# Optimization experiments

Measured on AMD Instinct MI355X. Metric: run time of the kernel, lower is better.

Reference implementation:

```python
import jax, jax.numpy as jnp
import numpy as np

EPS = float(jnp.finfo(jnp.float32).eps)  # torch.nn.RMSNorm default eps for fp32
TOP_K = 2


def rmsnorm(x, w):
    return x * jax.lax.rsqrt(jnp.mean(x * x, axis=-1, keepdims=True) + EPS) * w


def setup_inputs() -> dict:
    B, T, D_IN, D_MODEL, D_FF, D_OUT, E = 8, 1024, 1024, 1024, 4096, 1024, 8
    STD = 0.02
    key = jax.random.key(0)
    ks = jax.random.split(key, 8)
    return {
        "s": jax.random.normal(ks[0], (B, T, D_IN), dtype=jnp.float32),
        "W_in": STD * jax.random.normal(ks[1], (D_MODEL, D_IN), dtype=jnp.float32),
        "in_norm_w": jnp.ones((D_MODEL,), dtype=jnp.float32),
        "Wr": STD * jax.random.normal(ks[2], (E, D_MODEL), dtype=jnp.float32),
        "expert_bias": jnp.zeros((E,), dtype=jnp.float32),
        "Wg": STD * jax.random.normal(ks[3], (E, D_FF, D_MODEL), dtype=jnp.float32),
        "Wu": STD * jax.random.normal(ks[4], (E, D_FF, D_MODEL), dtype=jnp.float32),
        "Wd": STD * jax.random.normal(ks[5], (E, D_MODEL, D_FF), dtype=jnp.float32),
        "enorm_w": jnp.ones((E, D_MODEL), dtype=jnp.float32),
        "out_norm_w": jnp.ones((D_MODEL,), dtype=jnp.float32),
        "W_out": STD * jax.random.normal(ks[6], (D_OUT, D_MODEL), dtype=jnp.float32),
    }


def reference(s, W_in, in_norm_w, Wr, expert_bias, Wg, Wu, Wd, enorm_w, out_norm_w, W_out):
    B, T, _ = s.shape
    x = s.reshape(B * T, -1)                      # (N, d_in)
    h = rmsnorm(x @ W_in.T, in_norm_w)            # (N, d_model)

    # --- top-k router (DeepSeek-style bias for selection, orig logits for gates) ---
    logits = h @ Wr.T                              # (N, E)
    _, idx = jax.lax.top_k(logits + expert_bias, TOP_K)   # (N, k)
    sel = jnp.take_along_axis(logits, idx, axis=-1)
    g_topk = jax.nn.softmax(sel, axis=-1)
    N = logits.shape[0]
    gates = jnp.zeros_like(logits).at[jnp.arange(N)[:, None], idx].set(g_topk)

    # --- experts: gates are exactly 0 for unselected experts, so the dense
    # weighted sum equals the original masked gather/scatter combine ---
    out = jnp.zeros_like(h)
    for e in range(Wg.shape[0]):
        gate = jax.nn.silu(h @ Wg[e].T)            # (N, d_ff)
        up = h @ Wu[e].T
        oe = rmsnorm((gate * up) @ Wd[e].T, enorm_w[e])
        out = out + gates[:, e:e + 1] * oe

    s_hat = rmsnorm(out, out_norm_w) @ W_out.T     # (N, d_out)
    return s_hat.reshape(B, T, -1)
```

## Files before the change

### kernel.cpp

```cpp
#include <hip/hip_runtime.h>


#define NT      8192
#define DMODEL  1024
#define DFF     4096
#define NEXP    8
#define MAXROWS (NT * 2 + NEXP * 256)
#define RMS_EPS 1.1920928955078125e-07f

typedef __attribute__((ext_vector_type(8))) short bf16x8;
typedef __attribute__((ext_vector_type(4))) float f32x4;

__device__ __forceinline__ float bf2f(unsigned short u) {
  union { unsigned int i; float f; } c; c.i = ((unsigned int)u) << 16; return c.f;
}
__device__ __forceinline__ unsigned short f2bf(float f) {
  union { float f; unsigned int i; } c; c.f = f;
  unsigned int x = c.i;
  return (unsigned short)((x + 0x7FFFu + ((x >> 16) & 1u)) >> 16);
}

#define BARX() __builtin_amdgcn_s_barrier()
#define LGKM0() do { asm volatile("s_waitcnt lgkmcnt(0)" ::: "memory"); \
                     __builtin_amdgcn_sched_barrier(0); } while (0)
#define VMC(n)  do { asm volatile("s_waitcnt vmcnt(" #n ")" ::: "memory"); \
                     __builtin_amdgcn_sched_barrier(0); } while (0)

__global__ __launch_bounds__(256) void cast_bf16_kernel(
    const float* __restrict__ src, unsigned short* __restrict__ dst, long n) {
  long i = ((long)blockIdx.x * 256 + threadIdx.x) * 4;
  const long stride = (long)gridDim.x * 1024;
  for (; i < n; i += stride) {
    float4 v = *(const float4*)(src + i);
    ushort4 o;
    o.x = f2bf(v.x); o.y = f2bf(v.y); o.z = f2bf(v.z); o.w = f2bf(v.w);
    *(ushort4*)(dst + i) = o;
  }
}

__device__ __forceinline__ void async_cp16(const void* g, void* l) {
  __builtin_amdgcn_global_load_lds((const __attribute__((address_space(1))) void*)g,
                                   (__attribute__((address_space(3))) void*)l, 16, 0, 0);
}

template <int FUSED>
__global__ __launch_bounds__(512, 2) void gemm8ph(
    const unsigned short* __restrict__ A,
    const unsigned short* __restrict__ W0,
    const unsigned short* __restrict__ W1,
    void* __restrict__ Cv, void* __restrict__ Cv2,
    const int* __restrict__ offs,
    int K, int KT, size_t wstride) {
  const int gx = gridDim.x;
  const int nwg = gx * gridDim.y;
  int bid = blockIdx.y * gx + blockIdx.x;
  {
    const int q = nwg >> 3, r = nwg & 7;
    const int x = bid & 7, l = bid >> 3;
    bid = (x < r ? x * (q + 1) : r * (q + 1) + (x - r) * q) + l;
  }
  const int bx = bid % gx, by = bid / gx;

  const int row0 = bx * 256;
  if (row0 >= offs[NEXP]) return;
  int e = 0;
#pragma unroll
  for (int i = 1; i < NEXP; ++i) e += (row0 >= offs[i]) ? 1 : 0;

  __shared__ __align__(16) unsigned short lds[65536];

  const int t = threadIdx.x;
  const int lane = t & 63;
  const int wave = t >> 6;
  const int wm = wave >> 2, wn = wave & 3;
  const int lm = lane & 15, kq = lane >> 4;
  const int k0 = blockIdx.z * (KT << 6);

  const unsigned short* aP[2];
  const unsigned short* bP[2];
  int dl[2];
#pragma unroll
  for (int q = 0; q < 2; ++q) {
    const int L = q * 512 + t;
    const int row = L >> 2;
    const int kp = (t & 3) ^ ((row >> 1) & 3);
    dl[q] = L * 8;
    aP[q] = A + (size_t)(row0 + row) * K + kp * 8 + k0;
    if (FUSED) {
      const int f = by * 128 + ((row >> 6) << 5) + (row & 31);
      const unsigned short* wb = (row & 32) ? W1 : W0;
      bP[q] = wb + (size_t)e * wstride + (size_t)f * K + kp * 8 + k0;
    } else {
      bP[q] = W0 + (size_t)e * wstride + (size_t)(by * 256 + row) * K + kp * 8 + k0;
    }
  }

  int afo[8], bfo[4];
#pragma unroll
  for (int mi = 0; mi < 8; ++mi) {
    const int r = wm * 128 + mi * 16 + lm;
    afo[mi] = r * 32 + ((kq ^ ((r >> 1) & 3)) << 3);
  }
#pragma unroll
  for (int ni = 0; ni < 4; ++ni) {
    const int r = wn * 64 + ni * 16 + lm;
    bfo[ni] = 16384 + r * 32 + ((kq ^ ((r >> 1) & 3)) << 3);
  }

  f32x4 acc[8][4];
#pragma unroll
  for (int i = 0; i < 8; ++i)
#pragma unroll
    for (int j = 0; j < 4; ++j) acc[i][j] = (f32x4){0.f, 0.f, 0.f, 0.f};

  auto STG = [&](int tau, int ks, int isB) {
    const int roff = ((tau & 1) << 15) + (isB << 14) + (ks << 13);
    const int koff = (tau << 6) + (ks << 5);
#pragma unroll
    for (int q = 0; q < 2; ++q)
      async_cp16((isB ? bP[q] : aP[q]) + koff, lds + roff + dl[q]);
  };

  STG(0, 0, 0); STG(0, 0, 1); STG(0, 1, 0); STG(0, 1, 1);
  STG(1, 0, 0); STG(1, 0, 1); STG(1, 1, 0);
  VMC(6);
  BARX();

  for (int tau = 0; tau < KT; ++tau) {
    const int tb = (tau & 1) << 15;
    const bool s1 = (tau + 1 < KT), s2 = (tau + 2 < KT);
    bf16x8 af[8], bq0, bq1;

#pragma unroll
    for (int mi = 0; mi < 8; ++mi) af[mi] = *(const bf16x8*)(lds + tb + afo[mi]);
    bq0 = *(const bf16x8*)(lds + tb + bfo[0]);
    bq1 = *(const bf16x8*)(lds + tb + bfo[1]);
    if (s1) STG(tau + 1, 1, 1);
    BARX(); LGKM0();
    __builtin_amdgcn_s_setprio(1);
#pragma unroll
    for (int mi = 0; mi < 8; ++mi) {
      acc[mi][0] = __builtin_amdgcn_mfma_f32_16x16x32_bf16(af[mi], bq0, acc[mi][0], 0, 0, 0);
      acc[mi][1] = __builtin_amdgcn_mfma_f32_16x16x32_bf16(af[mi], bq1, acc[mi][1], 0, 0, 0);
    }
    __builtin_amdgcn_s_setprio(0);
    BARX();

    bq0 = *(const bf16x8*)(lds + tb + bfo[2]);
    bq1 = *(const bf16x8*)(lds + tb + bfo[3]);
    if (s2) STG(tau + 2, 0, 0);
    BARX(); LGKM0();
    __builtin_amdgcn_s_setprio(1);
#pragma unroll
    for (int mi = 0; mi < 8; ++mi) {
      acc[mi][2] = __builtin_amdgcn_mfma_f32_16x16x32_bf16(af[mi], bq0, acc[mi][2], 0, 0, 0);
      acc[mi][3] = __builtin_amdgcn_mfma_f32_16x16x32_bf16(af[mi], bq1, acc[mi][3], 0, 0, 0);
    }
    __builtin_amdgcn_s_setprio(0);
    BARX();

#pragma unroll
    for (int mi = 0; mi < 8; ++mi) af[mi] = *(const bf16x8*)(lds + tb + 8192 + afo[mi]);
    bq0 = *(const bf16x8*)(lds + tb + 8192 + bfo[0]);
    bq1 = *(const bf16x8*)(lds + tb + 8192 + bfo[1]);
    if (s2) STG(tau + 2, 0, 1);
    BARX(); LGKM0();
    __builtin_amdgcn_s_setprio(1);
#pragma unroll
    for (int mi = 0; mi < 8; ++mi) {
      acc[mi][0] = __builtin_amdgcn_mfma_f32_16x16x32_bf16(af[mi], bq0, acc[mi][0], 0, 0, 0);
      acc[mi][1] = __builtin_amdgcn_mfma_f32_16x16x32_bf16(af[mi], bq1, acc[mi][1], 0, 0, 0);
    }
    __builtin_amdgcn_s_setprio(0);
    BARX();

    bq0 = *(const bf16x8*)(lds + tb + 8192 + bfo[2]);
    bq1 = *(const bf16x8*)(lds + tb + 8192 + bfo[3]);
    if (s2) STG(tau + 2, 1, 0);
    BARX(); LGKM0();
    __builtin_amdgcn_s_setprio(1);
#pragma unroll
    for (int mi = 0; mi < 8; ++mi) {
      acc[mi][2] = __builtin_amdgcn_mfma_f32_16x16x32_bf16(af[mi], bq0, acc[mi][2], 0, 0, 0);
      acc[mi][3] = __builtin_amdgcn_mfma_f32_16x16x32_bf16(af[mi], bq1, acc[mi][3], 0, 0, 0);
    }
    __builtin_amdgcn_s_setprio(0);
    if (tau + 3 <= KT) { VMC(6); }
    else if (tau + 2 == KT) { VMC(0); }
    BARX();
  }

  const long rbase = (long)row0 + wm * 128 + kq * 4;
  if (FUSED) {
    unsigned short* Hc = (unsigned short*)Cv;
    const int cb = by * 128 + wn * 32 + lm;
#pragma unroll
    for (int mi = 0; mi < 8; ++mi)
#pragma unroll
      for (int ni = 0; ni < 2; ++ni)
#pragma unroll
        for (int rr = 0; rr < 4; ++rr) {
          const float g = acc[mi][ni][rr];
          const float u = acc[mi][ni + 2][rr];
          const float h = g / (1.f + expf(-g)) * u;
          Hc[(rbase + mi * 16 + rr) * (long)DFF + cb + ni * 16] = f2bf(h);
        }
  } else {
    float* Cp = blockIdx.z ? (float*)Cv2 : (float*)Cv;
    const int cb = by * 256 + wn * 64 + lm;
#pragma unroll
    for (int mi = 0; mi < 8; ++mi)
#pragma unroll
      for (int ni = 0; ni < 4; ++ni)
#pragma unroll
        for (int rr = 0; rr < 4; ++rr)
          Cp[(rbase + mi * 16 + rr) * (long)DMODEL + cb + ni * 16] = acc[mi][ni][rr];
  }
}

template <int BM, int BN, int WM, int WN, int WRITE_BF16, int FUSE_SILU, int GROUPED>
__global__ __launch_bounds__(WM * WN * 64, 2) void gemm2ph(
    const unsigned short* __restrict__ A,
    const unsigned short* __restrict__ W,
    void* __restrict__ Cv,
    const int* __restrict__ offs,
    int N, int K, size_t wstride) {
  constexpr int NTHR = WM * WN * 64;
  constexpr int TM = BM / WM;
  constexpr int TN = BN / WN;
  constexpr int AM = TM / 16;
  constexpr int AN = TN / 16;
  constexpr int LA = BM * 8 / NTHR;
  constexpr int LB = BN * 8 / NTHR;

  const int gx = gridDim.x;
  const int nwg = gx * gridDim.y;
  int bid = blockIdx.y * gx + blockIdx.x;
  {
    const int q = nwg >> 3, r = nwg & 7;
    const int x = bid & 7, l = bid >> 3;
    bid = (x < r ? x * (q + 1) : r * (q + 1) + (x - r) * q) + l;
  }
  const int bx = bid % gx;
  const int by = bid / gx;

  const int row0 = bx * BM;
  const unsigned short* Bp;
  if constexpr (GROUPED) {
    if (row0 >= offs[NEXP]) return;
    int e = 0;
#pragma unroll
    for (int i = 1; i < NEXP; ++i) e += (row0 >= offs[i]) ? 1 : 0;
    Bp = W + (size_t)e * wstride;
  } else {
    Bp = W;
  }

  __shared__ __align__(16) unsigned short As[2][BM * 64];
  __shared__ __align__(16) unsigned short Bs[2][BN * 64];

  const int tid = threadIdx.x;
  const int lane = tid & 63, wave = tid >> 6;
  const int wm = wave / WN, wn = wave % WN;
  const int lm = lane & 15, kq = lane >> 4;

  const long arow = row0;
  const long brow = (long)by * BN;

  const unsigned short* asrc[LA];
  unsigned short* adst[LA];
#pragma unroll
  for (int q = 0; q < LA; ++q) {
    const int c = q * NTHR + tid;
    asrc[q] = A + (arow + (c >> 3)) * (long)K + ((c & 7) << 3);
    adst[q] = &As[0][c * 8];
  }
  const unsigned short* bsrc[LB];
  unsigned short* bdst[LB];
#pragma unroll
  for (int q = 0; q < LB; ++q) {
    const int c = q * NTHR + tid;
    bsrc[q] = Bp + (brow + (c >> 3)) * (long)K + ((c & 7) << 3);
    bdst[q] = &Bs[0][c * 8];
  }

  f32x4 acc[AM][AN];
#pragma unroll
  for (int i = 0; i < AM; ++i)
#pragma unroll
    for (int j = 0; j < AN; ++j) acc[i][j] = (f32x4){0.f, 0.f, 0.f, 0.f};

  const int KT = K >> 6;

#pragma unroll
  for (int q = 0; q < LA; ++q) async_cp16(asrc[q], adst[q]);
#pragma unroll
  for (int q = 0; q < LB; ++q) async_cp16(bsrc[q], bdst[q]);
  __syncthreads();

  for (int kt = 0; kt < KT; ++kt) {
    const int cur = kt & 1;
    if (kt + 1 < KT) {
      const int koff = (kt + 1) << 6;
      const int ao = (cur ^ 1) * (BM * 64);
      const int bo = (cur ^ 1) * (BN * 64);
#pragma unroll
      for (int q = 0; q < LA; ++q) async_cp16(asrc[q] + koff, adst[q] + ao);
#pragma unroll
      for (int q = 0; q < LB; ++q) async_cp16(bsrc[q] + koff, bdst[q] + bo);
    }
    const unsigned short* Ab = As[cur];
    const unsigned short* Bb = Bs[cur];
#pragma unroll
    for (int ks = 0; ks < 2; ++ks) {
      bf16x8 af[AM], bfr[AN];
#pragma unroll
      for (int mi = 0; mi < AM; ++mi)
        af[mi] = *(const bf16x8*)(Ab + (wm * TM + mi * 16 + lm) * 64 + ks * 32 + kq * 8);
#pragma unroll
      for (int ni = 0; ni < AN; ++ni)
        bfr[ni] = *(const bf16x8*)(Bb + (wn * TN + ni * 16 + lm) * 64 + ks * 32 + kq * 8);
#pragma unroll
      for (int mi = 0; mi < AM; ++mi)
#pragma unroll
        for (int ni = 0; ni < AN; ++ni)
          acc[mi][ni] = __builtin_amdgcn_mfma_f32_16x16x32_bf16(af[mi], bfr[ni],
                                                                acc[mi][ni], 0, 0, 0);
    }
    __syncthreads();
  }

  const long rbase = arow + wm * TM + kq * 4;
  const long cbase = brow + wn * TN + lm;
#pragma unroll
  for (int mi = 0; mi < AM; ++mi)
#pragma unroll
    for (int ni = 0; ni < AN; ++ni)
#pragma unroll
      for (int r = 0; r < 4; ++r) {
        const long row = rbase + mi * 16 + r;
        const long col = cbase + ni * 16;
        float v = acc[mi][ni][r];
        if constexpr (FUSE_SILU) {
          const float g = bf2f(((const unsigned short*)Cv)[row * N + col]);
          v = g / (1.f + expf(-g)) * v;
        }
        if constexpr (WRITE_BF16) ((unsigned short*)Cv)[row * N + col] = f2bf(v);
        else                      ((float*)Cv)[row * N + col] = v;
      }
}

__global__ __launch_bounds__(256) void rmsnorm_kernel(
    const float* __restrict__ in, const float* __restrict__ w,
    unsigned short* __restrict__ out, float* __restrict__ invrms) {
  const int row = blockIdx.x;
  const int tid = threadIdx.x;
  const float4 xv = ((const float4*)(in + (long)row * DMODEL))[tid];
  float ss = xv.x * xv.x + xv.y * xv.y + xv.z * xv.z + xv.w * xv.w;
#pragma unroll
  for (int o = 32; o > 0; o >>= 1) ss += __shfl_xor(ss, o);
  __shared__ float red[4];
  if ((tid & 63) == 0) red[tid >> 6] = ss;
  __syncthreads();
  const float tot = red[0] + red[1] + red[2] + red[3];
  const float s = rsqrtf(tot * (1.f / DMODEL) + RMS_EPS);
  if (invrms != nullptr && tid == 0) invrms[row] = s;
  const float4 wv = ((const float4*)w)[tid];
  ushort4 o4;
  o4.x = f2bf(xv.x * s * wv.x);
  o4.y = f2bf(xv.y * s * wv.y);
  o4.z = f2bf(xv.z * s * wv.z);
  o4.w = f2bf(xv.w * s * wv.w);
  ((ushort4*)(out + (long)row * DMODEL))[tid] = o4;
}

__global__ __launch_bounds__(256) void router_prep_kernel(
    const float* __restrict__ Wr, const float* __restrict__ nw,
    const float* __restrict__ W_in, float* __restrict__ Wr2) {
  __shared__ float wr[NEXP * DMODEL];
  const int tid = threadIdx.x;
  for (int i = tid; i < NEXP * DMODEL; i += 256) wr[i] = Wr[i] * nw[i & (DMODEL - 1)];
  __syncthreads();
  const int kl = tid & 127;
  const int eb = (tid >> 7) * 4;
  const int kg = blockIdx.x * 128 + kl;
  float a0 = 0.f, a1 = 0.f, a2 = 0.f, a3 = 0.f;
  for (int j = 0; j < DMODEL; ++j) {
    const float wij = W_in[(long)j * DMODEL + kg];
    a0 += wr[(eb + 0) * DMODEL + j] * wij;
    a1 += wr[(eb + 1) * DMODEL + j] * wij;
    a2 += wr[(eb + 2) * DMODEL + j] * wij;
    a3 += wr[(eb + 3) * DMODEL + j] * wij;
  }
  Wr2[(eb + 0) * DMODEL + kg] = a0;
  Wr2[(eb + 1) * DMODEL + kg] = a1;
  Wr2[(eb + 2) * DMODEL + kg] = a2;
  Wr2[(eb + 3) * DMODEL + kg] = a3;
}

__global__ __launch_bounds__(64) void router_kernel(
    const float* __restrict__ x, const float* __restrict__ Wr2,
    const float* __restrict__ bias, const float* __restrict__ invrms,
    int* __restrict__ cnt, int* __restrict__ tok, float* __restrict__ gv) {
  const int row = blockIdx.x;
  const int lane = threadIdx.x;
  const float* xr = x + (long)row * DMODEL;
  float p[NEXP] = {0.f, 0.f, 0.f, 0.f, 0.f, 0.f, 0.f, 0.f};
  for (int k = lane; k < DMODEL; k += 64) {
    const float xv = xr[k];
#pragma unroll
    for (int e = 0; e < NEXP; ++e) p[e] += xv * Wr2[e * DMODEL + k];
  }
#pragma unroll
  for (int o = 32; o > 0; o >>= 1)
#pragma unroll
    for (int e = 0; e < NEXP; ++e) p[e] += __shfl_xor(p[e], o);
  if (lane == 0) {
    const float s = invrms[row];
    float logit[NEXP];
    float b0 = -1e30f, b1 = -1e30f;
    int i0 = 0, i1 = 0;
#pragma unroll
    for (int e = 0; e < NEXP; ++e) {
      logit[e] = p[e] * s;
      const float be = logit[e] + bias[e];
      if (be > b0)      { b1 = b0; i1 = i0; b0 = be; i0 = e; }
      else if (be > b1) { b1 = be; i1 = e; }
    }
    const float l0 = logit[i0], l1 = logit[i1];
    const float m = fmaxf(l0, l1);
    const float e0 = expf(l0 - m), e1 = expf(l1 - m);
    const float inv = 1.f / (e0 + e1);
    const int s0 = atomicAdd(&cnt[i0], 1);
    tok[i0 * NT + s0] = row;
    gv[i0 * NT + s0] = e0 * inv;
    const int s1 = atomicAdd(&cnt[i1], 1);
    tok[i1 * NT + s1] = row;
    gv[i1 * NT + s1] = e1 * inv;
  }
}

__global__ __launch_bounds__(256) void pad_kernel(
    const int* __restrict__ cnt, int* __restrict__ tok,
    int* __restrict__ pcnt, int* __restrict__ off) {
  __shared__ int sc[NEXP], sp[NEXP];
  const int tid = threadIdx.x;
  if (tid == 0) {
    int o = 0;
    for (int e = 0; e < NEXP; ++e) {
      const int c = cnt[e];
      const int p = (c + 255) & ~255;
      sc[e] = c; sp[e] = p;
      pcnt[e] = p; off[e] = o;
      o += p;
    }
    off[NEXP] = o;
  }
  __syncthreads();
  for (int e = 0; e < NEXP; ++e) {
    const int c = sc[e], p = sp[e];
    for (int s = c + tid; s < p; s += 256) tok[e * NT + s] = 0;
  }
}

__global__ __launch_bounds__(256) void gather_kernel(
    const unsigned short* __restrict__ hb, const int* __restrict__ tok,
    const int* __restrict__ offs, unsigned short* __restrict__ Ac) {
  const int r = blockIdx.x;
  if (r >= offs[NEXP]) return;
  int e = 0;
#pragma unroll
  for (int i = 1; i < NEXP; ++i) e += (r >= offs[i]) ? 1 : 0;
  const int src = tok[e * NT + (r - offs[e])];
  const ushort4* s4 = (const ushort4*)(hb + (long)src * DMODEL);
  ushort4* d4 = (ushort4*)(Ac + (long)r * DMODEL);
  d4[threadIdx.x] = s4[threadIdx.x];
}

__global__ __launch_bounds__(256) void expert_scatter(
    const float* __restrict__ oe0, const float* __restrict__ oe1,
    const float* __restrict__ enw,
    const int* __restrict__ tok, const float* __restrict__ gv,
    const int* __restrict__ cnt, const int* __restrict__ off,
    int e, float* __restrict__ acc) {
  const int s = blockIdx.x;
  if (s >= cnt[e]) return;
  const int row = tok[e * NT + s];
  const float g = gv[e * NT + s];
  const int tid = threadIdx.x;
  const long idx = ((long)off[e] + s) * DMODEL;
  const float4 x0 = ((const float4*)(oe0 + idx))[tid];
  const float4 x1 = ((const float4*)(oe1 + idx))[tid];
  float4 xv;
  xv.x = x0.x + x1.x; xv.y = x0.y + x1.y; xv.z = x0.z + x1.z; xv.w = x0.w + x1.w;
  float ss = xv.x * xv.x + xv.y * xv.y + xv.z * xv.z + xv.w * xv.w;
#pragma unroll
  for (int o = 32; o > 0; o >>= 1) ss += __shfl_xor(ss, o);
  __shared__ float red[4];
  if ((tid & 63) == 0) red[tid >> 6] = ss;
  __syncthreads();
  const float tot = red[0] + red[1] + red[2] + red[3];
  const float sc = rsqrtf(tot * (1.f / DMODEL) + RMS_EPS) * g;
  const float4 wv = ((const float4*)enw)[tid];
  float4* ap = (float4*)(acc + (long)row * DMODEL) + tid;
  float4 a = *ap;
  a.x += xv.x * sc * wv.x;
  a.y += xv.y * sc * wv.y;
  a.z += xv.z * sc * wv.z;
  a.w += xv.w * sc * wv.w;
  *ap = a;
}

extern "C" void kernel_launch(void* const* d_in, const int* in_sizes, int n_in,
                              void* d_out, int out_size, void* d_ws, size_t ws_size,
                              hipStream_t stream) {
  (void)in_sizes; (void)n_in; (void)out_size; (void)ws_size;
  const float* s_in  = (const float*)d_in[0];
  const float* W_in  = (const float*)d_in[1];
  const float* innw  = (const float*)d_in[2];
  const float* Wr    = (const float*)d_in[3];
  const float* ebias = (const float*)d_in[4];
  const float* Wg    = (const float*)d_in[5];
  const float* Wu    = (const float*)d_in[6];
  const float* Wd    = (const float*)d_in[7];
  const float* enw   = (const float*)d_in[8];
  const float* outnw = (const float*)d_in[9];
  const float* W_out = (const float*)d_in[10];
  float* out = (float*)d_out;

  char* base = (char*)d_ws;
  size_t off_b = 0;
  auto alloc = [&](size_t bytes) -> char* {
    char* p = base + off_b;
    off_b += (bytes + 255) & ~(size_t)255;
    return p;
  };
  unsigned short* xb    = (unsigned short*)alloc((size_t)NT * DMODEL * 2);
  unsigned short* Winb  = (unsigned short*)alloc((size_t)DMODEL * DMODEL * 2);
  unsigned short* Wgb   = (unsigned short*)alloc((size_t)NEXP * DFF * DMODEL * 2);
  unsigned short* Wub   = (unsigned short*)alloc((size_t)NEXP * DFF * DMODEL * 2);
  unsigned short* Wdb   = (unsigned short*)alloc((size_t)NEXP * DMODEL * DFF * 2);
  unsigned short* Woutb = (unsigned short*)alloc((size_t)DMODEL * DMODEL * 2);
  float*          hpre  = (float*)alloc((size_t)NT * DMODEL * 4);
  unsigned short* hb    = (unsigned short*)alloc((size_t)NT * DMODEL * 2);
  float*          invr  = (float*)alloc((size_t)NT * 4);
  float*          Wr2   = (float*)alloc((size_t)NEXP * DMODEL * 4);
  int*            cnt   = (int*)alloc((size_t)NEXP * 4);
  int*            pcnt  = (int*)alloc((size_t)NEXP * 4);
  int*            offs  = (int*)alloc((size_t)(NEXP + 1) * 4);
  int*            tok   = (int*)alloc((size_t)NEXP * NT * 4);
  float*          gv    = (float*)alloc((size_t)NEXP * NT * 4);
  unsigned short* Ac    = (unsigned short*)alloc((size_t)MAXROWS * DMODEL * 2);
  unsigned short* Hc    = (unsigned short*)alloc((size_t)MAXROWS * DFF * 2);
  float*          oec   = (float*)alloc((size_t)MAXROWS * DMODEL * 4);
  float*          accb  = hpre;
  unsigned short* yb    = xb;
  float*          oec2  = (float*)Wgb;

  hipMemsetAsync(cnt, 0, NEXP * 4, stream);
  cast_bf16_kernel<<<2048, 256, 0, stream>>>(s_in, xb, (long)NT * DMODEL);
  cast_bf16_kernel<<<2048, 256, 0, stream>>>(W_in, Winb, (long)DMODEL * DMODEL);
  cast_bf16_kernel<<<2048, 256, 0, stream>>>(Wg, Wgb, (long)NEXP * DFF * DMODEL);
  cast_bf16_kernel<<<2048, 256, 0, stream>>>(Wu, Wub, (long)NEXP * DFF * DMODEL);
  cast_bf16_kernel<<<2048, 256, 0, stream>>>(Wd, Wdb, (long)NEXP * DMODEL * DFF);
  cast_bf16_kernel<<<2048, 256, 0, stream>>>(W_out, Woutb, (long)DMODEL * DMODEL);

  gemm2ph<128, 128, 2, 2, 0, 0, 0><<<dim3(NT / 128, DMODEL / 128), 256, 0, stream>>>(
      xb, Winb, hpre, nullptr, DMODEL, DMODEL, 0);
  rmsnorm_kernel<<<NT, 256, 0, stream>>>(hpre, innw, hb, invr);
  hipMemsetAsync(accb, 0, (size_t)NT * DMODEL * 4, stream);

  router_prep_kernel<<<DMODEL / 128, 256, 0, stream>>>(Wr, innw, W_in, Wr2);
  router_kernel<<<NT, 64, 0, stream>>>(s_in, Wr2, ebias, invr, cnt, tok, gv);
  pad_kernel<<<1, 256, 0, stream>>>(cnt, tok, pcnt, offs);

  gather_kernel<<<MAXROWS, 256, 0, stream>>>(hb, tok, offs, Ac);

  gemm8ph<1><<<dim3(MAXROWS / 256, DFF / 128), 512, 0, stream>>>(
      Ac, Wgb, Wub, Hc, nullptr, offs, DMODEL, DMODEL / 64, (size_t)DFF * DMODEL);

  gemm8ph<0><<<dim3(MAXROWS / 256, DMODEL / 256, 2), 512, 0, stream>>>(
      Hc, Wdb, nullptr, oec, oec2, offs, DFF, 32, (size_t)DMODEL * DFF);

  for (int e = 0; e < NEXP; ++e)
    expert_scatter<<<NT, 256, 0, stream>>>(
        oec, oec2, enw + (size_t)e * DMODEL, tok, gv, cnt, offs, e, accb);

  rmsnorm_kernel<<<NT, 256, 0, stream>>>(accb, outnw, yb, nullptr);
  gemm2ph<128, 128, 2, 2, 0, 0, 0><<<dim3(NT / 128, DMODEL / 128), 256, 0, stream>>>(
      yb, Woutb, out, nullptr, DMODEL, DMODEL, 0);
}
```

Baseline: 1.416 ms.

## Fuse per-expert scatter and output RMSNorm into one per-token combine kernel

Replaces the eight per-expert scatter launches, the accumulator memset and the separate output RMSNorm with one combine kernel per token. The router now records each token's expert ids, slots and gates, so the combine kernel can gather its two expert rows and apply both norms in a single pass. This removes repeated read-modify-write traffic on the fp32 accumulator. The dense input and output projections also move from the 128x128 gemm2ph kernel to the 256-tile 8-wave gemm8ph kernel with grouping disabled. Using gemm8ph with z=0 means the full K range is handled, with KT=16 for K=1024.

```diff
diff --git a/kernel.cpp b/kernel.cpp
--- a/kernel.cpp
+++ b/kernel.cpp
@@ -43,7 +43,7 @@
                                    (__attribute__((address_space(3))) void*)l, 16, 0, 0);
 }
 
-template <int FUSED>
+template <int FUSED, int GROUPED>
 __global__ __launch_bounds__(512, 2) void gemm8ph(
     const unsigned short* __restrict__ A,
     const unsigned short* __restrict__ W0,
@@ -62,10 +62,12 @@
   const int bx = bid % gx, by = bid / gx;
 
   const int row0 = bx * 256;
-  if (row0 >= offs[NEXP]) return;
   int e = 0;
-#pragma unroll
-  for (int i = 1; i < NEXP; ++i) e += (row0 >= offs[i]) ? 1 : 0;
+  if constexpr (GROUPED) {
+    if (row0 >= offs[NEXP]) return;
+#pragma unroll
+    for (int i = 1; i < NEXP; ++i) e += (row0 >= offs[i]) ? 1 : 0;
+  }
 
   __shared__ __align__(16) unsigned short lds[65536];
 
@@ -218,138 +220,6 @@
   }
 }
 
-template <int BM, int BN, int WM, int WN, int WRITE_BF16, int FUSE_SILU, int GROUPED>
-__global__ __launch_bounds__(WM * WN * 64, 2) void gemm2ph(
-    const unsigned short* __restrict__ A,
-    const unsigned short* __restrict__ W,
-    void* __restrict__ Cv,
-    const int* __restrict__ offs,
-    int N, int K, size_t wstride) {
-  constexpr int NTHR = WM * WN * 64;
-  constexpr int TM = BM / WM;
-  constexpr int TN = BN / WN;
-  constexpr int AM = TM / 16;
-  constexpr int AN = TN / 16;
-  constexpr int LA = BM * 8 / NTHR;
-  constexpr int LB = BN * 8 / NTHR;
-
-  const int gx = gridDim.x;
-  const int nwg = gx * gridDim.y;
-  int bid = blockIdx.y * gx + blockIdx.x;
-  {
-    const int q = nwg >> 3, r = nwg & 7;
-    const int x = bid & 7, l = bid >> 3;
-    bid = (x < r ? x * (q + 1) : r * (q + 1) + (x - r) * q) + l;
-  }
-  const int bx = bid % gx;
-  const int by = bid / gx;
-
-  const int row0 = bx * BM;
-  const unsigned short* Bp;
-  if constexpr (GROUPED) {
-    if (row0 >= offs[NEXP]) return;
-    int e = 0;
-#pragma unroll
-    for (int i = 1; i < NEXP; ++i) e += (row0 >= offs[i]) ? 1 : 0;
-    Bp = W + (size_t)e * wstride;
-  } else {
-    Bp = W;
-  }
-
-  __shared__ __align__(16) unsigned short As[2][BM * 64];
-  __shared__ __align__(16) unsigned short Bs[2][BN * 64];
-
-  const int tid = threadIdx.x;
-  const int lane = tid & 63, wave = tid >> 6;
-  const int wm = wave / WN, wn = wave % WN;
-  const int lm = lane & 15, kq = lane >> 4;
-
-  const long arow = row0;
-  const long brow = (long)by * BN;
-
-  const unsigned short* asrc[LA];
-  unsigned short* adst[LA];
-#pragma unroll
-  for (int q = 0; q < LA; ++q) {
-    const int c = q * NTHR + tid;
-    asrc[q] = A + (arow + (c >> 3)) * (long)K + ((c & 7) << 3);
-    adst[q] = &As[0][c * 8];
-  }
-  const unsigned short* bsrc[LB];
-  unsigned short* bdst[LB];
-#pragma unroll
-  for (int q = 0; q < LB; ++q) {
-    const int c = q * NTHR + tid;
-    bsrc[q] = Bp + (brow + (c >> 3)) * (long)K + ((c & 7) << 3);
-    bdst[q] = &Bs[0][c * 8];
-  }
-
-  f32x4 acc[AM][AN];
-#pragma unroll
-  for (int i = 0; i < AM; ++i)
-#pragma unroll
-    for (int j = 0; j < AN; ++j) acc[i][j] = (f32x4){0.f, 0.f, 0.f, 0.f};
-
-  const int KT = K >> 6;
-
-#pragma unroll
-  for (int q = 0; q < LA; ++q) async_cp16(asrc[q], adst[q]);
-#pragma unroll
-  for (int q = 0; q < LB; ++q) async_cp16(bsrc[q], bdst[q]);
-  __syncthreads();
-
-  for (int kt = 0; kt < KT; ++kt) {
-    const int cur = kt & 1;
-    if (kt + 1 < KT) {
-      const int koff = (kt + 1) << 6;
-      const int ao = (cur ^ 1) * (BM * 64);
-      const int bo = (cur ^ 1) * (BN * 64);
-#pragma unroll
-      for (int q = 0; q < LA; ++q) async_cp16(asrc[q] + koff, adst[q] + ao);
-#pragma unroll
-      for (int q = 0; q < LB; ++q) async_cp16(bsrc[q] + koff, bdst[q] + bo);
-    }
-    const unsigned short* Ab = As[cur];
-    const unsigned short* Bb = Bs[cur];
-#pragma unroll
-    for (int ks = 0; ks < 2; ++ks) {
-      bf16x8 af[AM], bfr[AN];
-#pragma unroll
-      for (int mi = 0; mi < AM; ++mi)
-        af[mi] = *(const bf16x8*)(Ab + (wm * TM + mi * 16 + lm) * 64 + ks * 32 + kq * 8);
-#pragma unroll
-      for (int ni = 0; ni < AN; ++ni)
-        bfr[ni] = *(const bf16x8*)(Bb + (wn * TN + ni * 16 + lm) * 64 + ks * 32 + kq * 8);
-#pragma unroll
-      for (int mi = 0; mi < AM; ++mi)
-#pragma unroll
-        for (int ni = 0; ni < AN; ++ni)
-          acc[mi][ni] = __builtin_amdgcn_mfma_f32_16x16x32_bf16(af[mi], bfr[ni],
-                                                                acc[mi][ni], 0, 0, 0);
-    }
-    __syncthreads();
-  }
-
-  const long rbase = arow + wm * TM + kq * 4;
-  const long cbase = brow + wn * TN + lm;
-#pragma unroll
-  for (int mi = 0; mi < AM; ++mi)
-#pragma unroll
-    for (int ni = 0; ni < AN; ++ni)
-#pragma unroll
-      for (int r = 0; r < 4; ++r) {
-        const long row = rbase + mi * 16 + r;
-        const long col = cbase + ni * 16;
-        float v = acc[mi][ni][r];
-        if constexpr (FUSE_SILU) {
-          const float g = bf2f(((const unsigned short*)Cv)[row * N + col]);
-          v = g / (1.f + expf(-g)) * v;
-        }
-        if constexpr (WRITE_BF16) ((unsigned short*)Cv)[row * N + col] = f2bf(v);
-        else                      ((float*)Cv)[row * N + col] = v;
-      }
-}
-
 __global__ __launch_bounds__(256) void rmsnorm_kernel(
     const float* __restrict__ in, const float* __restrict__ w,
     unsigned short* __restrict__ out, float* __restrict__ invrms) {
@@ -401,7 +271,8 @@
 __global__ __launch_bounds__(64) void router_kernel(
     const float* __restrict__ x, const float* __restrict__ Wr2,
     const float* __restrict__ bias, const float* __restrict__ invrms,
-    int* __restrict__ cnt, int* __restrict__ tok, float* __restrict__ gv) {
+    int* __restrict__ cnt, int* __restrict__ tok,
+    int* __restrict__ te, int2* __restrict__ ts, float2* __restrict__ tg) {
   const int row = blockIdx.x;
   const int lane = threadIdx.x;
   const float* xr = x + (long)row * DMODEL;
@@ -433,16 +304,16 @@
     const float inv = 1.f / (e0 + e1);
     const int s0 = atomicAdd(&cnt[i0], 1);
     tok[i0 * NT + s0] = row;
-    gv[i0 * NT + s0] = e0 * inv;
     const int s1 = atomicAdd(&cnt[i1], 1);
     tok[i1 * NT + s1] = row;
-    gv[i1 * NT + s1] = e1 * inv;
+    te[row] = i0 | (i1 << 8);
+    ts[row] = make_int2(s0, s1);
+    tg[row] = make_float2(e0 * inv, e1 * inv);
   }
 }
 
 __global__ __launch_bounds__(256) void pad_kernel(
-    const int* __restrict__ cnt, int* __restrict__ tok,
-    int* __restrict__ pcnt, int* __restrict__ off) {
+    const int* __restrict__ cnt, int* __restrict__ tok, int* __restrict__ off) {
   __shared__ int sc[NEXP], sp[NEXP];
   const int tid = threadIdx.x;
   if (tid == 0) {
@@ -451,7 +322,7 @@
       const int c = cnt[e];
       const int p = (c + 255) & ~255;
       sc[e] = c; sp[e] = p;
-      pcnt[e] = p; off[e] = o;
+      off[e] = o;
       o += p;
     }
     off[NEXP] = o;
@@ -477,38 +348,70 @@
   d4[threadIdx.x] = s4[threadIdx.x];
 }
 
-__global__ __launch_bounds__(256) void expert_scatter(
+__global__ __launch_bounds__(256) void combine_kernel(
     const float* __restrict__ oe0, const float* __restrict__ oe1,
-    const float* __restrict__ enw,
-    const int* __restrict__ tok, const float* __restrict__ gv,
-    const int* __restrict__ cnt, const int* __restrict__ off,
-    int e, float* __restrict__ acc) {
-  const int s = blockIdx.x;
-  if (s >= cnt[e]) return;
-  const int row = tok[e * NT + s];
-  const float g = gv[e * NT + s];
+    const float* __restrict__ enw, const float* __restrict__ outnw,
+    const int* __restrict__ offs, const int* __restrict__ te,
+    const int2* __restrict__ ts, const float2* __restrict__ tg,
+    unsigned short* __restrict__ yb) {
+  const int row = blockIdx.x;
   const int tid = threadIdx.x;
-  const long idx = ((long)off[e] + s) * DMODEL;
-  const float4 x0 = ((const float4*)(oe0 + idx))[tid];
-  const float4 x1 = ((const float4*)(oe1 + idx))[tid];
-  float4 xv;
-  xv.x = x0.x + x1.x; xv.y = x0.y + x1.y; xv.z = x0.z + x1.z; xv.w = x0.w + x1.w;
-  float ss = xv.x * xv.x + xv.y * xv.y + xv.z * xv.z + xv.w * xv.w;
-#pragma unroll
-  for (int o = 32; o > 0; o >>= 1) ss += __shfl_xor(ss, o);
-  __shared__ float red[4];
-  if ((tid & 63) == 0) red[tid >> 6] = ss;
-  __syncthreads();
-  const float tot = red[0] + red[1] + red[2] + red[3];
-  const float sc = rsqrtf(tot * (1.f / DMODEL) + RMS_EPS) * g;
-  const float4 wv = ((const float4*)enw)[tid];
-  float4* ap = (float4*)(acc + (long)row * DMODEL) + tid;
-  float4 a = *ap;
-  a.x += xv.x * sc * wv.x;
-  a.y += xv.y * sc * wv.y;
-  a.z += xv.z * sc * wv.z;
-  a.w += xv.w * sc * wv.w;
-  *ap = a;
+  const int pe = te[row];
+  const int e0 = pe & 0xff, e1 = (pe >> 8) & 0xff;
+  const int2 sl = ts[row];
+  const float2 g = tg[row];
+  const long r0 = (long)(offs[e0] + sl.x) * DMODEL;
+  const long r1 = (long)(offs[e1] + sl.y) * DMODEL;
+
+  float4 a = ((const float4*)(oe0 + r0))[tid];
+  {
+    const float4 b = ((const float4*)(oe1 + r0))[tid];
+    a.x += b.x; a.y += b.y; a.z += b.z; a.w += b.w;
+  }
+  float4 c = ((const float4*)(oe0 + r1))[tid];
+  {
+    const float4 d = ((const float4*)(oe1 + r1))[tid];
+    c.x += d.x; c.y += d.y; c.z += d.z; c.w += d.w;
+  }
+  float s0 = a.x * a.x + a.y * a.y + a.z * a.z + a.w * a.w;
+  float s1 = c.x * c.x + c.y * c.y + c.z * c.z + c.w * c.w;
+#pragma unroll
+  for (int o = 32; o > 0; o >>= 1) {
+    s0 += __shfl_xor(s0, o);
+    s1 += __shfl_xor(s1, o);
+  }
+  __shared__ float red[8];
+  if ((tid & 63) == 0) { red[tid >> 6] = s0; red[4 + (tid >> 6)] = s1; }
+  __syncthreads();
+  s0 = red[0] + red[1] + red[2] + red[3];
+  s1 = red[4] + red[5] + red[6] + red[7];
+  const float n0 = rsqrtf(s0 * (1.f / DMODEL) + RMS_EPS) * g.x;
+  const float n1 = rsqrtf(s1 * (1.f / DMODEL) + RMS_EPS) * g.y;
+
+  const float4 w0 = ((const float4*)(enw + (size_t)e0 * DMODEL))[tid];
+  const float4 w1 = ((const float4*)(enw + (size_t)e1 * DMODEL))[tid];
+  float4 v;
+  v.x = a.x * n0 * w0.x + c.x * n1 * w1.x;
+  v.y = a.y * n0 * w0.y + c.y * n1 * w1.y;
+  v.z = a.z * n0 * w0.z + c.z * n1 * w1.z;
+  v.w = a.w * n0 * w0.w + c.w * n1 * w1.w;
+
+  float sv = v.x * v.x + v.y * v.y + v.z * v.z + v.w * v.w;
+#pragma unroll
+  for (int o = 32; o > 0; o >>= 1) sv += __shfl_xor(sv, o);
+  __syncthreads();
+  if ((tid & 63) == 0) red[tid >> 6] = sv;
+  __syncthreads();
+  sv = red[0] + red[1] + red[2] + red[3];
+  const float so = rsqrtf(sv * (1.f / DMODEL) + RMS_EPS);
+
+  const float4 wo = ((const float4*)outnw)[tid];
+  ushort4 o4;
+  o4.x = f2bf(v.x * so * wo.x);
+  o4.y = f2bf(v.y * so * wo.y);
+  o4.z = f2bf(v.z * so * wo.z);
+  o4.w = f2bf(v.w * so * wo.w);
+  ((ushort4*)(yb + (long)row * DMODEL))[tid] = o4;
 }
 
 extern "C" void kernel_launch(void* const* d_in, const int* in_sizes, int n_in,
@@ -546,14 +449,14 @@
   float*          invr  = (float*)alloc((size_t)NT * 4);
   float*          Wr2   = (float*)alloc((size_t)NEXP * DMODEL * 4);
   int*            cnt   = (int*)alloc((size_t)NEXP * 4);
-  int*            pcnt  = (int*)alloc((size_t)NEXP * 4);
   int*            offs  = (int*)alloc((size_t)(NEXP + 1) * 4);
   int*            tok   = (int*)alloc((size_t)NEXP * NT * 4);
-  float*          gv    = (float*)alloc((size_t)NEXP * NT * 4);
+  int*            te    = (int*)alloc((size_t)NT * 4);
+  int2*           ts    = (int2*)alloc((size_t)NT * 8);
+  float2*         tg    = (float2*)alloc((size_t)NT * 8);
   unsigned short* Ac    = (unsigned short*)alloc((size_t)MAXROWS * DMODEL * 2);
   unsigned short* Hc    = (unsigned short*)alloc((size_t)MAXROWS * DFF * 2);
   float*          oec   = (float*)alloc((size_t)MAXROWS * DMODEL * 4);
-  float*          accb  = hpre;
   unsigned short* yb    = xb;
   float*          oec2  = (float*)Wgb;
 
@@ -565,28 +468,25 @@
   cast_bf16_kernel<<<2048, 256, 0, stream>>>(Wd, Wdb, (long)NEXP * DMODEL * DFF);
   cast_bf16_kernel<<<2048, 256, 0, stream>>>(W_out, Woutb, (long)DMODEL * DMODEL);
 
-  gemm2ph<128, 128, 2, 2, 0, 0, 0><<<dim3(NT / 128, DMODEL / 128), 256, 0, stream>>>(
-      xb, Winb, hpre, nullptr, DMODEL, DMODEL, 0);
+  gemm8ph<0, 0><<<dim3(NT / 256, DMODEL / 256), 512, 0, stream>>>(
+      xb, Winb, nullptr, hpre, nullptr, nullptr, DMODEL, DMODEL / 64, 0);
   rmsnorm_kernel<<<NT, 256, 0, stream>>>(hpre, innw, hb, invr);
-  hipMemsetAsync(accb, 0, (size_t)NT * DMODEL * 4, stream);
 
   router_prep_kernel<<<DMODEL / 128, 256, 0, stream>>>(Wr, innw, W_in, Wr2);
-  router_kernel<<<NT, 64, 0, stream>>>(s_in, Wr2, ebias, invr, cnt, tok, gv);
-  pad_kernel<<<1, 256, 0, stream>>>(cnt, tok, pcnt, offs);
+  router_kernel<<<NT, 64, 0, stream>>>(s_in, Wr2, ebias, invr, cnt, tok, te, ts, tg);
+  pad_kernel<<<1, 256, 0, stream>>>(cnt, tok, offs);
 
   gather_kernel<<<MAXROWS, 256, 0, stream>>>(hb, tok, offs, Ac);
 
-  gemm8ph<1><<<dim3(MAXROWS / 256, DFF / 128), 512, 0, stream>>>(
+  gemm8ph<1, 1><<<dim3(MAXROWS / 256, DFF / 128), 512, 0, stream>>>(
       Ac, Wgb, Wub, Hc, nullptr, offs, DMODEL, DMODEL / 64, (size_t)DFF * DMODEL);
 
-  gemm8ph<0><<<dim3(MAXROWS / 256, DMODEL / 256, 2), 512, 0, stream>>>(
+  gemm8ph<0, 1><<<dim3(MAXROWS / 256, DMODEL / 256, 2), 512, 0, stream>>>(
       Hc, Wdb, nullptr, oec, oec2, offs, DFF, 32, (size_t)DMODEL * DFF);
 
-  for (int e = 0; e < NEXP; ++e)
-    expert_scatter<<<NT, 256, 0, stream>>>(
-        oec, oec2, enw + (size_t)e * DMODEL, tok, gv, cnt, offs, e, accb);
-
-  rmsnorm_kernel<<<NT, 256, 0, stream>>>(accb, outnw, yb, nullptr);
-  gemm2ph<128, 128, 2, 2, 0, 0, 0><<<dim3(NT / 128, DMODEL / 128), 256, 0, stream>>>(
-      yb, Woutb, out, nullptr, DMODEL, DMODEL, 0);
-}
+  combine_kernel<<<NT, 256, 0, stream>>>(
+      oec, oec2, enw, outnw, offs, te, ts, tg, yb);
+
+  gemm8ph<0, 0><<<dim3(NT / 256, DMODEL / 256), 512, 0, stream>>>(
+      yb, Woutb, nullptr, out, nullptr, nullptr, DMODEL, DMODEL / 64, 0);
+}
```

Result: faster. 1.375 ms (-2.9%).
